# Kernel tuning notes

Hardware: AMD Instinct MI355X
Metric: run time of the kernel (lower is better)

## Reference

```python
import jax, jax.numpy as jnp
import numpy as np

B, S, F, H, L = 4096, 512, 8, 10, 2


def setup_inputs() -> dict:
    key = jax.random.key(0)
    ks = jax.random.split(key, 12)
    bound = 1.0 / np.sqrt(H)  # PyTorch LSTM/Linear init scale
    u = lambda k, shape: jax.random.uniform(k, shape, jnp.float32, -bound, bound)
    return {
        "input_tensor": jax.random.normal(ks[0], (B, S, F), jnp.float32),
        "hidden": jnp.zeros((L, B, H), jnp.float32),
        "cell": jnp.zeros((L, B, H), jnp.float32),
        # layer 0 (input size F), layer 1 (input size H); gate order i,f,g,o
        "W_ih0": u(ks[1], (4 * H, F)), "W_hh0": u(ks[2], (4 * H, H)),
        "b_ih0": u(ks[3], (4 * H,)),   "b_hh0": u(ks[4], (4 * H,)),
        "W_ih1": u(ks[5], (4 * H, H)), "W_hh1": u(ks[6], (4 * H, H)),
        "b_ih1": u(ks[7], (4 * H,)),   "b_hh1": u(ks[8], (4 * H,)),
        "W_fc": u(ks[9], (1, H)),      "b_fc": u(ks[10], (1,)),
    }


def _lstm_layer(x_sbf, h0, c0, W_ih, W_hh, b_ih, b_hh):
    # x_sbf: [S, B, Fin]; h0,c0: [B, H]. Returns hs [S,B,H], (hT, cT).
    b = b_ih + b_hh

    def step(carry, x):
        h, c = carry
        gates = x @ W_ih.T + h @ W_hh.T + b  # [B, 4H]
        i, f, g, o = jnp.split(gates, 4, axis=-1)
        c = jax.nn.sigmoid(f) * c + jax.nn.sigmoid(i) * jnp.tanh(g)
        h = jax.nn.sigmoid(o) * jnp.tanh(c)
        return (h, c), h

    (hT, cT), hs = jax.lax.scan(step, (h0, c0), x_sbf)
    return hs, hT, cT


def reference(input_tensor, hidden, cell,
              W_ih0, W_hh0, b_ih0, b_hh0,
              W_ih1, W_hh1, b_ih1, b_hh1,
              W_fc, b_fc):
    x = jnp.transpose(input_tensor, (1, 0, 2))  # [S, B, F]
    hs0, h0T, c0T = _lstm_layer(x, hidden[0], cell[0], W_ih0, W_hh0, b_ih0, b_hh0)
    hs1, h1T, c1T = _lstm_layer(hs0, hidden[1], cell[1], W_ih1, W_hh1, b_ih1, b_hh1)
    out = hs1[-1]                      # last timestep, [B, H]
    out_regression = out @ W_fc.T + b_fc  # [B, 1]
    hidden_out = jnp.stack([h0T, h1T])
    cell_out = jnp.stack([c0T, c1T])
    return out_regression, hidden_out, cell_out
```

## Files before the change

### kernel.cpp

```cpp
#include <hip/hip_runtime.h>


typedef __fp16 v2h __attribute__((ext_vector_type(2)));
typedef __fp16 v8h __attribute__((ext_vector_type(8)));
struct h4 { v2h a, b, c, d; };

#define L2E 1.4426950408889634f

__device__ __forceinline__ v2h pkh(float a, float b) {
    return __builtin_amdgcn_cvt_pkrtz(a, b);
}
__device__ __forceinline__ float bpermf(int baddr, float v) {
    int r = __builtin_amdgcn_ds_bpermute(baddr, __builtin_bit_cast(int, v));
    return __builtin_bit_cast(float, r);
}

#define SIGM(a)  __builtin_amdgcn_rcpf(1.0f + __builtin_amdgcn_exp2f(-(a)))
#define TANHP(a) fmaf(-2.0f, __builtin_amdgcn_rcpf(1.0f + __builtin_amdgcn_exp2f(a)), 1.0f)
#define DOT2(acc, w, v) (acc) = __builtin_amdgcn_fdot2((w), (v), (acc), false)

#define READROW(PTR, H)                                                      \
    { v8h w0_ = *(const v8h*)(PTR);                                          \
      v2h w1_ = *(const v2h*)((PTR) + 8);                                    \
      h4 q_ = __builtin_bit_cast(h4, w0_);                                   \
      H[0]=q_.a; H[1]=q_.b; H[2]=q_.c; H[3]=q_.d; H[4]=w1_; }

__global__ __launch_bounds__(256, 2)
void lstm2_r17(const float* __restrict__ x,
               const float* __restrict__ hid,
               const float* __restrict__ cel,
               const float* __restrict__ Wih0, const float* __restrict__ Whh0,
               const float* __restrict__ bih0, const float* __restrict__ bhh0,
               const float* __restrict__ Wih1, const float* __restrict__ Whh1,
               const float* __restrict__ bih1, const float* __restrict__ bhh1,
               const float* __restrict__ Wfc,  const float* __restrict__ bfc,
               float* __restrict__ out)
{
    __shared__ __attribute__((aligned(16))) __fp16 h0buf[32][6][24];
    __shared__ __attribute__((aligned(16))) __fp16 h1buf[6][24];
    __shared__ float fcb[6][10];

    const int tid  = threadIdx.x;
    const int lane = tid & 63;
    const int uwid = __builtin_amdgcn_readfirstlane(tid >> 6);
    int grp = lane / 20;
    int l20 = lane - grp * 20;
    if (lane >= 60) { grp = 2; l20 = 19; }
    const int  ju       = (l20 < 10) ? l20 : l20 - 10;
    const bool unitlane = (l20 < 10);
    const int  eIw = (uwid & 1) * 3 + grp;
    const int  e   = blockIdx.x * 6 + eIw;
    const int  ec  = (e < 4095) ? e : 4095;
    const int  baddr = ((l20 < 10) ? (lane + 10) : lane) * 4;

    const float alpha2 = unitlane ? 2.0f : 1.0f;
    const float beta2  = unitlane ? -1.0f : 0.0f;
    const float scB    = unitlane ? 2.0f * L2E : L2E;
    const int   rA = l20, rB = 20 + l20;

    if (uwid < 2) {
        v2h wxA[4], wxB[4], whA[5], whB[5];
        #pragma unroll
        for (int k = 0; k < 4; ++k) {
            wxA[k] = pkh(Wih0[rA*8+2*k]*L2E, Wih0[rA*8+2*k+1]*L2E);
            wxB[k] = pkh(Wih0[rB*8+2*k]*scB, Wih0[rB*8+2*k+1]*scB);
        }
        #pragma unroll
        for (int k = 0; k < 5; ++k) {
            whA[k] = pkh(Whh0[rA*10+2*k]*L2E, Whh0[rA*10+2*k+1]*L2E);
            whB[k] = pkh(Whh0[rB*10+2*k]*scB, Whh0[rB*10+2*k+1]*scB);
        }
        const float bA = (bih0[rA] + bhh0[rA]) * L2E;
        const float bB = (bih0[rB] + bhh0[rB]) * scB;

        v2h hv[5];
        #pragma unroll
        for (int k = 0; k < 5; ++k) hv[k] = pkh(hid[ec*10+2*k], hid[ec*10+2*k+1]);
        float cc = cel[ec * 10 + ju];
        float hj = 0.0f;

        __fp16* const wbase = &h0buf[0][eIw][0];
        __fp16* const wlane = wbase + l20;

        const float4* __restrict__ xp4 = reinterpret_cast<const float4*>(x + (size_t)ec * 4096);
        float4 xb0[2], xb1[2], xb2[2], xb3[2];
        xb0[0]=xp4[0]; xb0[1]=xp4[1];  xb1[0]=xp4[2]; xb1[1]=xp4[3];
        xb2[0]=xp4[4]; xb2[1]=xp4[5];  xb3[0]=xp4[6]; xb3[1]=xp4[7];

        float axA[2], axB[2];
        {
            v2h x0=pkh(xb0[0].x,xb0[0].y), x1=pkh(xb0[0].z,xb0[0].w);
            v2h x2=pkh(xb0[1].x,xb0[1].y), x3=pkh(xb0[1].z,xb0[1].w);
            xb0[0]=xp4[8]; xb0[1]=xp4[9];
            float nA=bA, nB=bB;
            DOT2(nA,wxA[0],x0); DOT2(nB,wxB[0],x0);
            DOT2(nA,wxA[1],x1); DOT2(nB,wxB[1],x1);
            DOT2(nA,wxA[2],x2); DOT2(nB,wxB[2],x2);
            DOT2(nA,wxA[3],x3); DOT2(nB,wxB[3],x3);
            axA[0]=nA; axB[0]=nB;
        }

#define L0STEP(S, XB, DOREF, PC, PN)                                         \
        {                                                                    \
            v2h x0=pkh(XB[0].x,XB[0].y), x1=pkh(XB[0].z,XB[0].w);            \
            v2h x2=pkh(XB[1].x,XB[1].y), x3=pkh(XB[1].z,XB[1].w);            \
            if (DOREF) { XB[0]=xr[2*((S)+5)]; XB[1]=xr[2*((S)+5)+1]; }       \
            float nA=bA, nB=bB;                                              \
            DOT2(nA,wxA[0],x0); DOT2(nB,wxB[0],x0);                          \
            DOT2(nA,wxA[1],x1); DOT2(nB,wxB[1],x1);                          \
            DOT2(nA,wxA[2],x2); DOT2(nB,wxB[2],x2);                          \
            DOT2(nA,wxA[3],x3); DOT2(nB,wxB[3],x3);                          \
            axA[PN]=nA; axB[PN]=nB;                                          \
            float aA=axA[PC], aB=axB[PC];                                    \
            DOT2(aA,whA[0],hv[0]); DOT2(aB,whB[0],hv[0]);                    \
            DOT2(aA,whA[1],hv[1]); DOT2(aB,whB[1],hv[1]);                    \
            DOT2(aA,whA[2],hv[2]); DOT2(aB,whB[2],hv[2]);                    \
            DOT2(aA,whA[3],hv[3]); DOT2(aB,whB[3],hv[3]);                    \
            DOT2(aA,whA[4],hv[4]); DOT2(aB,whB[4],hv[4]);                    \
            float r1 = SIGM(aA);                                             \
            float r2 = __builtin_amdgcn_rcpf(1.0f + __builtin_amdgcn_exp2f(-aB)); \
            float act2 = fmaf(alpha2, r2, beta2);                            \
            float ig = r1 * act2;                                            \
            float sf = bpermf(baddr, r1);                                    \
            float so = bpermf(baddr, act2);                                  \
            cc = fmaf(sf, cc, ig);                                           \
            hj = so * TANHP((2.0f*L2E) * cc);                                \
            wlane[(S)*144] = (__fp16)hj;                                     \
            READROW(wbase + (S)*144, hv)                                     \
        }

#define L0HALF1(RF)                                                          \
            L0STEP(0,  xb1, 1,  0, 1)  L0STEP(1,  xb2, 1,  1, 0)             \
            L0STEP(2,  xb3, 1,  0, 1)  L0STEP(3,  xb0, 1,  1, 0)             \
            L0STEP(4,  xb1, 1,  0, 1)  L0STEP(5,  xb2, 1,  1, 0)             \
            L0STEP(6,  xb3, 1,  0, 1)  L0STEP(7,  xb0, 1,  1, 0)             \
            L0STEP(8,  xb1, 1,  0, 1)  L0STEP(9,  xb2, 1,  1, 0)             \
            L0STEP(10, xb3, 1,  0, 1)  L0STEP(11, xb0, 1,  1, 0)             \
            L0STEP(12, xb1, 1,  0, 1)  L0STEP(13, xb2, 1,  1, 0)             \
            L0STEP(14, xb3, 1,  0, 1)  L0STEP(15, xb0, RF, 1, 0)

        const float4* __restrict__ xr = xp4;
        for (int it = 0; it < 15; ++it) {
            L0HALF1(1)
            __syncthreads();
            L0STEP(16, xb1, 1, 0, 1)  L0STEP(17, xb2, 1, 1, 0)
            L0STEP(18, xb3, 1, 0, 1)  L0STEP(19, xb0, 1, 1, 0)
            L0STEP(20, xb1, 1, 0, 1)  L0STEP(21, xb2, 1, 1, 0)
            L0STEP(22, xb3, 1, 0, 1)  L0STEP(23, xb0, 1, 1, 0)
            L0STEP(24, xb1, 1, 0, 1)  L0STEP(25, xb2, 1, 1, 0)
            L0STEP(26, xb3, 1, 0, 1)  L0STEP(27, xb0, 1, 1, 0)
            L0STEP(28, xb1, 1, 0, 1)  L0STEP(29, xb2, 1, 1, 0)
            L0STEP(30, xb3, 1, 0, 1)  L0STEP(31, xb0, 1, 1, 0)
            __syncthreads();
            xr += 64;
        }
        L0HALF1(1)
        __syncthreads();
        L0STEP(16, xb1, 1, 0, 1)  L0STEP(17, xb2, 1, 1, 0)
        L0STEP(18, xb3, 1, 0, 1)  L0STEP(19, xb0, 1, 1, 0)
        L0STEP(20, xb1, 1, 0, 1)  L0STEP(21, xb2, 1, 1, 0)
        L0STEP(22, xb3, 1, 0, 1)  L0STEP(23, xb0, 1, 1, 0)
        L0STEP(24, xb1, 1, 0, 1)  L0STEP(25, xb2, 1, 1, 0)
        L0STEP(26, xb3, 1, 0, 1)  L0STEP(27, xb0, 0, 1, 0)
        L0STEP(28, xb1, 0, 0, 1)  L0STEP(29, xb2, 0, 1, 0)
        L0STEP(30, xb3, 0, 0, 1)  L0STEP(31, xb0, 0, 1, 0)
        __syncthreads();
#undef L0STEP
#undef L0HALF1

        __syncthreads();
        if (unitlane && e < 4096) {
            out[4096          + e * 10 + ju] = hj;
            out[4096 + 81920  + e * 10 + ju] = cc;
        }

    } else {
        v2h wiA[5], wiB[5], whA[5], whB[5];
        #pragma unroll
        for (int k = 0; k < 5; ++k) {
            wiA[k] = pkh(Wih1[rA*10+2*k]*L2E, Wih1[rA*10+2*k+1]*L2E);
            wiB[k] = pkh(Wih1[rB*10+2*k]*scB, Wih1[rB*10+2*k+1]*scB);
            whA[k] = pkh(Whh1[rA*10+2*k]*L2E, Whh1[rA*10+2*k+1]*L2E);
            whB[k] = pkh(Whh1[rB*10+2*k]*scB, Whh1[rB*10+2*k+1]*scB);
        }
        const float bA = (bih1[rA] + bhh1[rA]) * L2E;
        const float bB = (bih1[rB] + bhh1[rB]) * scB;
        const float wfc = Wfc[ju];

        v2h hv[5];
        #pragma unroll
        for (int k = 0; k < 5; ++k) hv[k] = pkh(hid[40960+ec*10+2*k], hid[40960+ec*10+2*k+1]);
        float cc = cel[40960 + ec * 10 + ju];
        float hj = 0.0f;

        const __fp16* const rbase = &h0buf[0][eIw][0];
        __fp16* const h1w  = &h1buf[eIw][0];
        __fp16* const h1wl = h1w + l20;

        v2h prA[5], prB[5];
        float ax0A, ax0B, ax1A, ax1B;

#define L1RD(PR, S)  READROW(rbase + (S)*144, PR)
#define L1DOTS(PR, AXA, AXB)                                                 \
        {                                                                    \
            float nA=bA, nB=bB;                                              \
            DOT2(nA,wiA[0],PR[0]); DOT2(nB,wiB[0],PR[0]);                    \
            DOT2(nA,wiA[1],PR[1]); DOT2(nB,wiB[1],PR[1]);                    \
            DOT2(nA,wiA[2],PR[2]); DOT2(nB,wiB[2],PR[2]);                    \
            DOT2(nA,wiA[3],PR[3]); DOT2(nB,wiB[3],PR[3]);                    \
            DOT2(nA,wiA[4],PR[4]); DOT2(nB,wiB[4],PR[4]);                    \
            AXA=nA; AXB=nB;                                                  \
        }
#define L1CORE(AXA, AXB)                                                     \
        {                                                                    \
            float aA=AXA, aB=AXB;                                            \
            DOT2(aA,whA[0],hv[0]); DOT2(aB,whB[0],hv[0]);                    \
            DOT2(aA,whA[1],hv[1]); DOT2(aB,whB[1],hv[1]);                    \
            DOT2(aA,whA[2],hv[2]); DOT2(aB,whB[2],hv[2]);                    \
            DOT2(aA,whA[3],hv[3]); DOT2(aB,whB[3],hv[3]);                    \
            DOT2(aA,whA[4],hv[4]); DOT2(aB,whB[4],hv[4]);                    \
            float r1 = SIGM(aA);                                             \
            float r2 = __builtin_amdgcn_rcpf(1.0f + __builtin_amdgcn_exp2f(-aB)); \
            float act2 = fmaf(alpha2, r2, beta2);                            \
            float ig = r1 * act2;                                            \
            float sf = bpermf(baddr, r1);                                    \
            float so = bpermf(baddr, act2);                                  \
            cc = fmaf(sf, cc, ig);                                           \
            hj = so * TANHP((2.0f*L2E) * cc);                                \
            h1wl[0] = (__fp16)hj;                                            \
            READROW(h1w, hv)                                                 \
        }

#define L1HALF(W)                                                            \
        L1RD(prA, (W)+0)                                                     \
        L1RD(prB, (W)+1)  L1DOTS(prA, ax0A, ax0B)                            \
        L1RD(prA, (W)+2)  L1DOTS(prB, ax1A, ax1B)  L1CORE(ax0A, ax0B)        \
        L1RD(prB, (W)+3)  L1DOTS(prA, ax0A, ax0B)  L1CORE(ax1A, ax1B)        \
        L1RD(prA, (W)+4)  L1DOTS(prB, ax1A, ax1B)  L1CORE(ax0A, ax0B)        \
        L1RD(prB, (W)+5)  L1DOTS(prA, ax0A, ax0B)  L1CORE(ax1A, ax1B)        \
        L1RD(prA, (W)+6)  L1DOTS(prB, ax1A, ax1B)  L1CORE(ax0A, ax0B)        \
        L1RD(prB, (W)+7)  L1DOTS(prA, ax0A, ax0B)  L1CORE(ax1A, ax1B)        \
        L1RD(prA, (W)+8)  L1DOTS(prB, ax1A, ax1B)  L1CORE(ax0A, ax0B)        \
        L1RD(prB, (W)+9)  L1DOTS(prA, ax0A, ax0B)  L1CORE(ax1A, ax1B)        \
        L1RD(prA, (W)+10) L1DOTS(prB, ax1A, ax1B)  L1CORE(ax0A, ax0B)        \
        L1RD(prB, (W)+11) L1DOTS(prA, ax0A, ax0B)  L1CORE(ax1A, ax1B)        \
        L1RD(prA, (W)+12) L1DOTS(prB, ax1A, ax1B)  L1CORE(ax0A, ax0B)        \
        L1RD(prB, (W)+13) L1DOTS(prA, ax0A, ax0B)  L1CORE(ax1A, ax1B)        \
        L1RD(prA, (W)+14) L1DOTS(prB, ax1A, ax1B)  L1CORE(ax0A, ax0B)        \
        L1RD(prB, (W)+15) L1DOTS(prA, ax0A, ax0B)  L1CORE(ax1A, ax1B)        \
                          L1DOTS(prB, ax1A, ax1B)  L1CORE(ax0A, ax0B)        \
                                                   L1CORE(ax1A, ax1B)

        for (int it = 0; it < 16; ++it) {
            __syncthreads();
            L1HALF(0)
            __syncthreads();
            L1HALF(16)
        }
#undef L1HALF
#undef L1RD
#undef L1DOTS
#undef L1CORE

        if (unitlane) fcb[eIw][ju] = hj * wfc;
        __syncthreads();
        if (l20 == 0 && e < 4096) {
            float p = bfc[0];
            #pragma unroll
            for (int k = 0; k < 10; ++k) p += fcb[eIw][k];
            out[e] = p;
        }
        if (unitlane && e < 4096) {
            out[4096 + 40960  + e * 10 + ju] = hj;
            out[4096 + 122880 + e * 10 + ju] = cc;
        }
    }
}

extern "C" void kernel_launch(void* const* d_in, const int* in_sizes, int n_in,
                              void* d_out, int out_size, void* d_ws, size_t ws_size,
                              hipStream_t stream) {
    const float* x    = (const float*)d_in[0];
    const float* hid  = (const float*)d_in[1];
    const float* cel  = (const float*)d_in[2];
    const float* Wih0 = (const float*)d_in[3];
    const float* Whh0 = (const float*)d_in[4];
    const float* bih0 = (const float*)d_in[5];
    const float* bhh0 = (const float*)d_in[6];
    const float* Wih1 = (const float*)d_in[7];
    const float* Whh1 = (const float*)d_in[8];
    const float* bih1 = (const float*)d_in[9];
    const float* bhh1 = (const float*)d_in[10];
    const float* Wfc  = (const float*)d_in[11];
    const float* bfc  = (const float*)d_in[12];

    hipLaunchKernelGGL(lstm2_r17, dim3(683), dim3(256), 0, stream,
                       x, hid, cel, Wih0, Whh0, bih0, bhh0,
                       Wih1, Whh1, bih1, bhh1, Wfc, bfc,
                       (float*)d_out);
}
```

Baseline: 159.6 us.

## Replace block-wide barriers with per-pair LDS flag handshakes between layer waves

Replaces the __syncthreads barriers between the layer-0 producer waves and layer-1 consumer waves with workgroup-scope acquire/release flags in LDS. Each wave pair (one layer-0 wave and one layer-1 wave) synchronises independently, so the two pairs no longer stall each other at full-block barriers. The cost is spin-waiting with s_sleep polling. There is also a correctness risk: the fcb reduction lost its barrier, and lane 0 publishes without any intra-wave ordering guarantee for LDS writes made by other lanes.

```diff
diff --git a/kernel.cpp b/kernel.cpp
--- a/kernel.cpp
+++ b/kernel.cpp
@@ -13,6 +13,14 @@
 __device__ __forceinline__ float bpermf(int baddr, float v) {
     int r = __builtin_amdgcn_ds_bpermute(baddr, __builtin_bit_cast(int, v));
     return __builtin_bit_cast(float, r);
+}
+__device__ __forceinline__ void wg_wait_ge(int* flag, int target) {
+    while (__hip_atomic_load(flag, __ATOMIC_ACQUIRE, __HIP_MEMORY_SCOPE_WORKGROUP) < target)
+        __builtin_amdgcn_s_sleep(2);
+}
+__device__ __forceinline__ void wg_publish(int* flag, int v, int lane) {
+    if (lane == 0)
+        __hip_atomic_store(flag, v, __ATOMIC_RELEASE, __HIP_MEMORY_SCOPE_WORKGROUP);
 }
 
 #define SIGM(a)  __builtin_amdgcn_rcpf(1.0f + __builtin_amdgcn_exp2f(-(a)))
@@ -26,7 +34,7 @@
       H[0]=q_.a; H[1]=q_.b; H[2]=q_.c; H[3]=q_.d; H[4]=w1_; }
 
 __global__ __launch_bounds__(256, 2)
-void lstm2_r17(const float* __restrict__ x,
+void lstm2_r18(const float* __restrict__ x,
                const float* __restrict__ hid,
                const float* __restrict__ cel,
                const float* __restrict__ Wih0, const float* __restrict__ Whh0,
@@ -39,6 +47,8 @@
     __shared__ __attribute__((aligned(16))) __fp16 h0buf[32][6][24];
     __shared__ __attribute__((aligned(16))) __fp16 h1buf[6][24];
     __shared__ float fcb[6][10];
+    __shared__ int s_prog[2];
+    __shared__ int s_cons[2];
 
     const int tid  = threadIdx.x;
     const int lane = tid & 63;
@@ -51,12 +61,16 @@
     const int  eIw = (uwid & 1) * 3 + grp;
     const int  e   = blockIdx.x * 6 + eIw;
     const int  ec  = (e < 4095) ? e : 4095;
+    const int  pair = uwid & 1;
     const int  baddr = ((l20 < 10) ? (lane + 10) : lane) * 4;
 
     const float alpha2 = unitlane ? 2.0f : 1.0f;
     const float beta2  = unitlane ? -1.0f : 0.0f;
     const float scB    = unitlane ? 2.0f * L2E : L2E;
     const int   rA = l20, rB = 20 + l20;
+
+    if (tid < 2) { s_prog[tid] = 0; s_cons[tid] = 0; }
+    __syncthreads();
 
     if (uwid < 2) {
         v2h wxA[4], wxB[4], whA[5], whB[5];
@@ -141,8 +155,10 @@
 
         const float4* __restrict__ xr = xp4;
         for (int it = 0; it < 15; ++it) {
+            wg_wait_ge(&s_cons[pair], 32*it - 16);
             L0HALF1(1)
-            __syncthreads();
+            wg_publish(&s_prog[pair], 32*it + 16, lane);
+            wg_wait_ge(&s_cons[pair], 32*it);
             L0STEP(16, xb1, 1, 0, 1)  L0STEP(17, xb2, 1, 1, 0)
             L0STEP(18, xb3, 1, 0, 1)  L0STEP(19, xb0, 1, 1, 0)
             L0STEP(20, xb1, 1, 0, 1)  L0STEP(21, xb2, 1, 1, 0)
@@ -151,11 +167,13 @@
             L0STEP(26, xb3, 1, 0, 1)  L0STEP(27, xb0, 1, 1, 0)
             L0STEP(28, xb1, 1, 0, 1)  L0STEP(29, xb2, 1, 1, 0)
             L0STEP(30, xb3, 1, 0, 1)  L0STEP(31, xb0, 1, 1, 0)
-            __syncthreads();
+            wg_publish(&s_prog[pair], 32*it + 32, lane);
             xr += 64;
         }
+        wg_wait_ge(&s_cons[pair], 32*15 - 16);
         L0HALF1(1)
-        __syncthreads();
+        wg_publish(&s_prog[pair], 496, lane);
+        wg_wait_ge(&s_cons[pair], 480);
         L0STEP(16, xb1, 1, 0, 1)  L0STEP(17, xb2, 1, 1, 0)
         L0STEP(18, xb3, 1, 0, 1)  L0STEP(19, xb0, 1, 1, 0)
         L0STEP(20, xb1, 1, 0, 1)  L0STEP(21, xb2, 1, 1, 0)
@@ -164,11 +182,10 @@
         L0STEP(26, xb3, 1, 0, 1)  L0STEP(27, xb0, 0, 1, 0)
         L0STEP(28, xb1, 0, 0, 1)  L0STEP(29, xb2, 0, 1, 0)
         L0STEP(30, xb3, 0, 0, 1)  L0STEP(31, xb0, 0, 1, 0)
-        __syncthreads();
+        wg_publish(&s_prog[pair], 512, lane);
 #undef L0STEP
 #undef L0HALF1
 
-        __syncthreads();
         if (unitlane && e < 4096) {
             out[4096          + e * 10 + ju] = hj;
             out[4096 + 81920  + e * 10 + ju] = cc;
@@ -252,10 +269,12 @@
                                                    L1CORE(ax1A, ax1B)
 
         for (int it = 0; it < 16; ++it) {
-            __syncthreads();
+            wg_wait_ge(&s_prog[pair], 32*it + 16);
             L1HALF(0)
-            __syncthreads();
+            wg_publish(&s_cons[pair], 32*it + 16, lane);
+            wg_wait_ge(&s_prog[pair], 32*it + 32);
             L1HALF(16)
+            wg_publish(&s_cons[pair], 32*it + 32, lane);
         }
 #undef L1HALF
 #undef L1RD
@@ -263,7 +282,6 @@
 #undef L1CORE
 
         if (unitlane) fcb[eIw][ju] = hj * wfc;
-        __syncthreads();
         if (l20 == 0 && e < 4096) {
             float p = bfc[0];
             #pragma unroll
@@ -294,7 +312,7 @@
     const float* Wfc  = (const float*)d_in[11];
     const float* bfc  = (const float*)d_in[12];
 
-    hipLaunchKernelGGL(lstm2_r17, dim3(683), dim3(256), 0, stream,
+    hipLaunchKernelGGL(lstm2_r18, dim3(683), dim3(256), 0, stream,
                        x, hid, cel, Wih0, Whh0, bih0, bhh0,
                        Wih1, Whh1, bih1, bhh1, Wfc, bfc,
                        (float*)d_out);
```

Result: faster. 156.0 us (-2.3%).
